# Kernel tuning notes

Measured on AMD Instinct MI355X. Metric: run time of the kernel, lower is better.

## Reference

```python
import jax, jax.numpy as jnp
import numpy as np

B, T, N = 8, 500, 4096
FRAC_EXC = 0.8
# CSV-derived physiological constants (seconds, mV, GOhm)
TAU_SYN_E, TAU_SYN_I = 0.005, 0.01
TAU_MEM_E, TAU_MEM_I = 0.02, 0.02
U_REST_E, U_REST_I = -65.0, -65.0
THETA_E, THETA_I = -50.0, -50.0
U_RESET_E, U_RESET_I = -65.0, -65.0
R_E, R_I = 0.1, 0.1


def setup_inputs() -> dict:
    key = jax.random.key(0)
    kw, = jax.random.split(key, 1)
    n_exc = int(N * FRAC_EXC)
    neuron_types = jnp.where(jnp.arange(N) < n_exc, 1, -1).astype(jnp.int32)
    # connectome weights: non-negative synapse counts; inhibitory presynaptic rows negative
    W = jnp.abs(jax.random.normal(kw, (N, N), jnp.float32)) * 0.01
    W = W * jnp.where(neuron_types == 1, 1.0, -1.0)[:, None]
    initial_v = jnp.broadcast_to(
        jnp.where(neuron_types == 1, U_REST_E, U_REST_I).astype(jnp.float32)[None, :], (B, N)
    ) + jnp.zeros((B, N), jnp.float32)
    return {
        "n_steps": T,
        "delta_t": jnp.float32(1.0),
        "neuron_types": neuron_types,
        "recurrent_weights": W,
        "E_weight": jnp.float32(1.5),
        "I_weight": jnp.float32(6.0),
        "initial_v": initial_v,
        "initial_I_exc": jnp.zeros((B, N), jnp.float32),
        "initial_I_inh": jnp.zeros((B, N), jnp.float32),
    }


def reference(n_steps, delta_t, neuron_types, recurrent_weights, E_weight, I_weight,
              initial_v, initial_I_exc, initial_I_inh):
    dt = delta_t * 0.001  # ms -> s
    alpha_E = jnp.exp(-dt / TAU_SYN_E)
    alpha_I = jnp.exp(-dt / TAU_SYN_I)
    beta_E = jnp.exp(-dt / TAU_MEM_E)
    beta_I = jnp.exp(-dt / TAU_MEM_I)

    is_exc = (neuron_types == 1)
    exc_mask = is_exc.astype(jnp.float32)  # (N,)
    # per-neuron (postsynaptic) constants, equivalent to the exc/inh index split
    beta = jnp.where(is_exc, beta_E, beta_I)
    U_rest = jnp.where(is_exc, U_REST_E, U_REST_I)
    theta = jnp.where(is_exc, THETA_E, THETA_I)
    U_reset = jnp.where(is_exc, U_RESET_E, U_RESET_I)
    R = jnp.where(is_exc, R_E, R_I)
    drive = R * (1.0 - beta)  # (N,)

    # column scaling by postsynaptic-column neuron type, exactly as in source
    scale = jnp.where(is_exc, E_weight, I_weight)
    W_scaled = recurrent_weights * scale[None, :]  # (N, N)

    def step(carry, _):
        v, I_exc, I_inh = carry  # each (B, N)
        I_total = I_exc + I_inh
        v = U_rest + (v - U_rest) * beta + I_total * drive
        s = (v >= theta).astype(v.dtype)
        v = v * (1.0 - s) + U_reset * s
        I_exc = I_exc * alpha_E + (s * exc_mask) @ W_scaled
        I_inh = I_inh * alpha_I + (s * (1.0 - exc_mask)) @ W_scaled
        return (v, I_exc, I_inh), (s, v, I_exc, I_inh)

    init = (initial_v, initial_I_exc, initial_I_inh)
    _, (all_s, all_v, all_I_exc, all_I_inh) = jax.lax.scan(step, init, None, length=int(n_steps))
    # (T, B, N) -> (B, T, N)
    tr = lambda x: jnp.transpose(x, (1, 0, 2))
    return tr(all_s), tr(all_v), tr(all_I_exc), tr(all_I_inh)
```

## Files before the change

kernel.cpp:

```cpp
#include <hip/hip_runtime.h>
#include <math.h>

#define TAU_SYN_E 0.005f
#define TAU_SYN_I 0.01f
#define TAU_MEM   0.02f
#define U_REST    (-65.0f)
#define THETA     (-50.0f)
#define U_RESET   (-65.0f)
#define R_CONST   0.1f

#define NO_SPIKE 0x7FFFFFFF

__global__ void lif_init_tfirst(int* tf, int nb) {
    int i = threadIdx.x + blockIdx.x * blockDim.x;
    if (i < nb) tf[i] = NO_SPIKE;
}

__global__ __launch_bounds__(64) void lif_indep(
    const int* __restrict__ n_steps_p,
    const float* __restrict__ delta_t_p,
    const float* __restrict__ init_v,
    const float* __restrict__ init_Ie,
    const float* __restrict__ init_Ii,
    float* __restrict__ out,
    int* __restrict__ tf,
    int B, int N)
{
    const int T = n_steps_p[0];
    const float dt = delta_t_p[0] * 0.001f;
    const float aE    = expf(-dt / TAU_SYN_E);
    const float aI    = expf(-dt / TAU_SYN_I);
    const float beta  = expf(-dt / TAU_MEM);
    const float drive = R_CONST * (1.0f - beta);

    int gid = blockIdx.x * blockDim.x + threadIdx.x;
    if (gid >= B * N) return;
    int b = gid / N;
    int n = gid - b * N;

    float v  = init_v[gid];
    float Ie = init_Ie[gid];
    float Ii = init_Ii[gid];

    size_t span = (size_t)B * (size_t)T * (size_t)N;
    float* __restrict__ out_s = out;
    float* __restrict__ out_v = out + span;
    float* __restrict__ out_e = out + 2 * span;
    float* __restrict__ out_i = out + 3 * span;

    size_t idx = (size_t)b * (size_t)T * (size_t)N + (size_t)n;
    bool spiked = false;

    for (int t = 0; t < T; ++t) {
        float Itot = Ie + Ii;
        v = U_REST + (v - U_REST) * beta + Itot * drive;
        float s = (v >= THETA) ? 1.0f : 0.0f;
        if (v >= THETA) {
            v = U_RESET;
            if (!spiked) { spiked = true; atomicMin(&tf[b], t); }
        }
        Ie *= aE;
        Ii *= aI;
        out_s[idx] = s;
        out_v[idx] = v;
        out_e[idx] = Ie;
        out_i[idx] = Ii;
        idx += (size_t)N;
    }
}

__global__ __launch_bounds__(1024) void lif_fixup(
    const int* __restrict__ n_steps_p,
    const float* __restrict__ delta_t_p,
    const int* __restrict__ types,
    const float* __restrict__ W,
    const float* __restrict__ Ew_p,
    const float* __restrict__ Iw_p,
    const float* __restrict__ init_v,
    const float* __restrict__ init_Ie,
    const float* __restrict__ init_Ii,
    float* __restrict__ out,
    const int* __restrict__ tf,
    int B, int N)
{
    const int b = blockIdx.x;
    if (tf[b] == NO_SPIKE) return;

    const int T = n_steps_p[0];
    const float dt = delta_t_p[0] * 0.001f;
    const float aE    = expf(-dt / TAU_SYN_E);
    const float aI    = expf(-dt / TAU_SYN_I);
    const float beta  = expf(-dt / TAU_MEM);
    const float drive = R_CONST * (1.0f - beta);
    const float Ew = Ew_p[0];
    const float Iw = Iw_p[0];

    const int NPT = (N + blockDim.x - 1) / blockDim.x;

    __shared__ int cnt;
    __shared__ int slist[4096];

    float v[8], Ie[8], Ii[8], sc[8];
    int   nn[8];
    for (int k = 0; k < NPT; ++k) {
        int n = threadIdx.x + k * blockDim.x;
        nn[k] = n;
        if (n < N) {
            v[k]  = init_v[(size_t)b * N + n];
            Ie[k] = init_Ie[(size_t)b * N + n];
            Ii[k] = init_Ii[(size_t)b * N + n];
            sc[k] = (types[n] == 1) ? Ew : Iw;
        }
    }

    size_t span = (size_t)B * (size_t)T * (size_t)N;
    float* __restrict__ out_s = out;
    float* __restrict__ out_v = out + span;
    float* __restrict__ out_e = out + 2 * span;
    float* __restrict__ out_i = out + 3 * span;

    for (int t = 0; t < T; ++t) {
        if (threadIdx.x == 0) cnt = 0;
        __syncthreads();

        for (int k = 0; k < NPT; ++k) {
            if (nn[k] >= N) continue;
            float Itot = Ie[k] + Ii[k];
            float vv = U_REST + (v[k] - U_REST) * beta + Itot * drive;
            float s = (vv >= THETA) ? 1.0f : 0.0f;
            if (vv >= THETA) {
                vv = U_RESET;
                int p = atomicAdd(&cnt, 1);
                slist[p] = nn[k];
            }
            v[k] = vv;
            size_t idx = (size_t)b * (size_t)T * N + (size_t)t * N + nn[k];
            out_s[idx] = s;
            out_v[idx] = vv;
        }
        __syncthreads();

        int c = cnt;
        for (int k = 0; k < NPT; ++k) {
            if (nn[k] >= N) continue;
            float accE = 0.0f, accI = 0.0f;
            for (int q = 0; q < c; ++q) {
                int j = slist[q];
                float w = W[(size_t)j * N + nn[k]];
                if (types[j] == 1) accE += w; else accI += w;
            }
            Ie[k] = Ie[k] * aE + accE * sc[k];
            Ii[k] = Ii[k] * aI + accI * sc[k];
            size_t idx = (size_t)b * (size_t)T * N + (size_t)t * N + nn[k];
            out_e[idx] = Ie[k];
            out_i[idx] = Ii[k];
        }
        __syncthreads();
    }
}

extern "C" void kernel_launch(void* const* d_in, const int* in_sizes, int n_in,
                              void* d_out, int out_size, void* d_ws, size_t ws_size,
                              hipStream_t stream) {
    const int*   n_steps = (const int*)d_in[0];
    const float* delta_t = (const float*)d_in[1];
    const int*   types   = (const int*)d_in[2];
    const float* W       = (const float*)d_in[3];
    const float* Ew      = (const float*)d_in[4];
    const float* Iw      = (const float*)d_in[5];
    const float* init_v  = (const float*)d_in[6];
    const float* init_Ie = (const float*)d_in[7];
    const float* init_Ii = (const float*)d_in[8];
    float* out = (float*)d_out;

    const int N = in_sizes[2];
    const int B = in_sizes[6] / N;
    int* tf = (int*)d_ws;

    hipLaunchKernelGGL(lif_init_tfirst, dim3(1), dim3(64), 0, stream, tf, B);

    const int total = B * N;
    hipLaunchKernelGGL(lif_indep, dim3((total + 63) / 64), dim3(64), 0, stream,
                       n_steps, delta_t, init_v, init_Ie, init_Ii, out, tf, B, N);

    hipLaunchKernelGGL(lif_fixup, dim3(B), dim3(1024), 0, stream,
                       n_steps, delta_t, types, W, Ew, Iw,
                       init_v, init_Ie, init_Ii, out, tf, B, N);
}
```

Measured before the change: 317.3 us.

## Parallelize no-spike LIF trajectory across time chunks using closed-form state

The independent (no-recurrence) LIF pass now splits the time axis into chunks of 10 steps. Each block computes its chunk's starting state in closed form from powers of the decay constants, then steps forward, using float4 vectorized loads and stores. This exposes far more parallelism than one thread per neuron looping over all 500 steps, and widens the stores. The closed form only holds until the first spike, and the later fixup kernel rewrites batches that do spike. Rounding differs slightly from sequential stepping.

```diff
diff --git a/kernel.cpp b/kernel.cpp
--- a/kernel.cpp
+++ b/kernel.cpp
@@ -10,13 +10,14 @@
 #define R_CONST   0.1f
 
 #define NO_SPIKE 0x7FFFFFFF
+#define TCHUNK 10
 
 __global__ void lif_init_tfirst(int* tf, int nb) {
     int i = threadIdx.x + blockIdx.x * blockDim.x;
     if (i < nb) tf[i] = NO_SPIKE;
 }
 
-__global__ __launch_bounds__(64) void lif_indep(
+__global__ __launch_bounds__(256) void lif_chunks(
     const int* __restrict__ n_steps_p,
     const float* __restrict__ delta_t_p,
     const float* __restrict__ init_v,
@@ -24,7 +25,7 @@
     const float* __restrict__ init_Ii,
     float* __restrict__ out,
     int* __restrict__ tf,
-    int B, int N)
+    int B, int N, int nChunks, int nBlkN)
 {
     const int T = n_steps_p[0];
     const float dt = delta_t_p[0] * 0.001f;
@@ -33,14 +34,42 @@
     const float beta  = expf(-dt / TAU_MEM);
     const float drive = R_CONST * (1.0f - beta);
 
-    int gid = blockIdx.x * blockDim.x + threadIdx.x;
-    if (gid >= B * N) return;
-    int b = gid / N;
-    int n = gid - b * N;
-
-    float v  = init_v[gid];
-    float Ie = init_Ie[gid];
-    float Ii = init_Ii[gid];
+    int blk = blockIdx.x;
+    int bn  = blk % nBlkN;
+    int tmp = blk / nBlkN;
+    int c   = tmp % nChunks;
+    int b   = tmp / nChunks;
+
+    int n = bn * (blockDim.x * 4) + threadIdx.x * 4;
+    if (n + 3 >= N + 4) return;
+    if (n + 3 >= N) return;
+
+    const int t0 = c * TCHUNK;
+    if (t0 >= T) return;
+    const int t1 = (t0 + TCHUNK < T) ? (t0 + TCHUNK) : T;
+
+    size_t base = (size_t)b * N + n;
+    float4 v0  = *(const float4*)&init_v [base];
+    float4 Ie0 = *(const float4*)&init_Ie[base];
+    float4 Ii0 = *(const float4*)&init_Ii[base];
+
+    const float pE = powf(aE,   (float)t0);
+    const float pI = powf(aI,   (float)t0);
+    const float pB = powf(beta, (float)t0);
+    const float gE = drive * (pE - pB) / (aE - beta);
+    const float gI = drive * (pI - pB) / (aI - beta);
+
+    float v[4], Ie[4], Ii[4];
+    {
+        const float* v0p  = (const float*)&v0;
+        const float* Iep  = (const float*)&Ie0;
+        const float* Iip  = (const float*)&Ii0;
+        for (int k = 0; k < 4; ++k) {
+            Ie[k] = Iep[k] * pE;
+            Ii[k] = Iip[k] * pI;
+            v[k]  = U_REST + (v0p[k] - U_REST) * pB + Iep[k] * gE + Iip[k] * gI;
+        }
+    }
 
     size_t span = (size_t)B * (size_t)T * (size_t)N;
     float* __restrict__ out_s = out;
@@ -48,24 +77,29 @@
     float* __restrict__ out_e = out + 2 * span;
     float* __restrict__ out_i = out + 3 * span;
 
-    size_t idx = (size_t)b * (size_t)T * (size_t)N + (size_t)n;
     bool spiked = false;
-
-    for (int t = 0; t < T; ++t) {
-        float Itot = Ie + Ii;
-        v = U_REST + (v - U_REST) * beta + Itot * drive;
-        float s = (v >= THETA) ? 1.0f : 0.0f;
-        if (v >= THETA) {
-            v = U_RESET;
-            if (!spiked) { spiked = true; atomicMin(&tf[b], t); }
-        }
-        Ie *= aE;
-        Ii *= aI;
-        out_s[idx] = s;
-        out_v[idx] = v;
-        out_e[idx] = Ie;
-        out_i[idx] = Ii;
-        idx += (size_t)N;
+    for (int t = t0; t < t1; ++t) {
+        float4 sv, vv, ev, iv;
+        float* svp = (float*)&sv; float* vvp = (float*)&vv;
+        float* evp = (float*)&ev; float* ivp = (float*)&iv;
+        for (int k = 0; k < 4; ++k) {
+            float Itot = Ie[k] + Ii[k];
+            float vn = U_REST + (v[k] - U_REST) * beta + Itot * drive;
+            float s = (vn >= THETA) ? 1.0f : 0.0f;
+            if (vn >= THETA) {
+                vn = U_RESET;
+                if (!spiked) { spiked = true; atomicMin(&tf[b], t); }
+            }
+            v[k] = vn;
+            Ie[k] *= aE;
+            Ii[k] *= aI;
+            svp[k] = s; vvp[k] = vn; evp[k] = Ie[k]; ivp[k] = Ii[k];
+        }
+        size_t idx = ((size_t)b * T + t) * (size_t)N + n;
+        *(float4*)&out_s[idx] = sv;
+        *(float4*)&out_v[idx] = vv;
+        *(float4*)&out_e[idx] = ev;
+        *(float4*)&out_i[idx] = iv;
     }
 }
 
@@ -175,13 +209,17 @@
 
     const int N = in_sizes[2];
     const int B = in_sizes[6] / N;
+    const int T = out_size / (4 * B * N);
     int* tf = (int*)d_ws;
 
     hipLaunchKernelGGL(lif_init_tfirst, dim3(1), dim3(64), 0, stream, tf, B);
 
-    const int total = B * N;
-    hipLaunchKernelGGL(lif_indep, dim3((total + 63) / 64), dim3(64), 0, stream,
-                       n_steps, delta_t, init_v, init_Ie, init_Ii, out, tf, B, N);
+    const int nChunks = (T + TCHUNK - 1) / TCHUNK;
+    const int nBlkN   = (N + 1023) / 1024;
+    const int nBlocks = B * nChunks * nBlkN;
+    hipLaunchKernelGGL(lif_chunks, dim3(nBlocks), dim3(256), 0, stream,
+                       n_steps, delta_t, init_v, init_Ie, init_Ii, out, tf,
+                       B, N, nChunks, nBlkN);
 
     hipLaunchKernelGGL(lif_fixup, dim3(B), dim3(1024), 0, stream,
                        n_steps, delta_t, types, W, Ew, Iw,
```

After: 316.7 us. Within noise of the previous version (-0.2%).
